# Optimization experiments

Measured on AMD Instinct MI355X. Metric: run time of the kernel, lower is better.

## Reference

```python
import jax, jax.numpy as jnp
import numpy as np

B, S, D = 2, 2048, 768
H, DK, F = 12, 64, 3072
LN_EPS = 1e-5


def setup_inputs() -> dict:
    key = jax.random.key(0)
    ks = jax.random.split(key, 8)
    w = lambda k, shape: jax.random.normal(k, shape, dtype=jnp.float32) * 0.02
    return {
        "x": jax.random.normal(ks[0], (B, S, D), dtype=jnp.float32),
        "wq_w": w(ks[1], (H, D, DK)), "wq_b": jnp.zeros((H, DK), jnp.float32),
        "wk_w": w(ks[2], (H, D, DK)), "wk_b": jnp.zeros((H, DK), jnp.float32),
        "wv_w": w(ks[3], (H, D, DK)), "wv_b": jnp.zeros((H, DK), jnp.float32),
        "wo_w": w(ks[4], (H * DK, D)), "wo_b": jnp.zeros((D,), jnp.float32),
        "ln_g": jnp.ones((D,), jnp.float32), "ln_b": jnp.zeros((D,), jnp.float32),
        "w1": w(ks[5], (D, F)), "b1": jnp.zeros((F,), jnp.float32),
        "w2": w(ks[6], (F, D)), "b2": jnp.zeros((D,), jnp.float32),
    }


def layer_norm(x, g, b):
    mu = jnp.mean(x, axis=-1, keepdims=True)
    var = jnp.mean(jnp.square(x - mu), axis=-1, keepdims=True)
    return (x - mu) * jax.lax.rsqrt(var + LN_EPS) * g + b


def reference(x, wq_w, wq_b, wk_w, wk_b, wv_w, wv_b, wo_w, wo_b,
              ln_g, ln_b, w1, b1, w2, b2):
    dk = wq_w.shape[-1]
    x_res = x
    h = layer_norm(x, ln_b=ln_b, g=ln_g, b=ln_b) if False else layer_norm(x, ln_g, ln_b)
    # per-head QKV (all heads batched via einsum): [B,H,S,DK]
    q = jnp.einsum("bsd,hdk->bhsk", h, wq_w) + wq_b[None, :, None, :]
    k = jnp.einsum("bsd,hdk->bhsk", h, wk_w) + wk_b[None, :, None, :]
    v = jnp.einsum("bsd,hdk->bhsk", h, wv_w) + wv_b[None, :, None, :]
    scores = jnp.einsum("bhqk,bhsk->bhqs", q, k) / jnp.sqrt(jnp.float32(dk))
    attn = jax.nn.softmax(scores, axis=-1)
    o = jnp.einsum("bhqs,bhsk->bhqk", attn, v)  # [B,H,S,DK]
    Bx, Hx, Sx, Dkx = o.shape
    o = o.transpose(0, 2, 1, 3).reshape(Bx, Sx, Hx * Dkx)  # concat heads
    y = o @ wo_w + wo_b + x_res  # residual 1
    y_res = y
    z = layer_norm(y, ln_g, ln_b)
    z = jax.nn.gelu(z @ w1 + b1, approximate=False) @ w2 + b2
    return z + y_res
```

## Files before the change

### kernel.cpp

```cpp
#include <hip/hip_runtime.h>
#include <hip/hip_bf16.h>
#include <math.h>

typedef __bf16 bf16_t;
typedef __bf16 bf16x8 __attribute__((ext_vector_type(8)));
typedef __bf16 bf16x4 __attribute__((ext_vector_type(4)));
typedef float f32x4 __attribute__((ext_vector_type(4)));

#define MFMA_B16(a, b, c) __builtin_amdgcn_mfma_f32_16x16x32_bf16((a), (b), (c), 0, 0, 0)

static constexpr int Bn = 2, Sn = 2048, Dn = 768, Hn = 12, Fn = 3072;
static constexpr int NTOK = Bn * Sn;
#define QSCALE 0.18033688011112042f

__device__ __forceinline__ void gl_lds16(const bf16_t* g, void* lds) {
  __builtin_amdgcn_global_load_lds(
      (const __attribute__((address_space(1))) uint32_t*)g,
      (__attribute__((address_space(3))) uint32_t*)lds, 16, 0, 0);
}

__global__ __launch_bounds__(256) void k_prep(const float* __restrict__ wq, const float* __restrict__ wk,
                                              const float* __restrict__ wv, const float* __restrict__ wo,
                                              const float* __restrict__ w1, const float* __restrict__ w2,
                                              const float* __restrict__ bq, const float* __restrict__ bk,
                                              const float* __restrict__ bv,
                                              bf16_t* __restrict__ WqkvT, bf16_t* __restrict__ WoT,
                                              bf16_t* __restrict__ W1T, bf16_t* __restrict__ W2T,
                                              float* __restrict__ QKVB) {
  int t = blockIdx.x;
  if (t >= 1728) {
    for (int i = threadIdx.x; i < 2304; i += 256)
      QKVB[i] = i < 768 ? bq[i] : (i < 1536 ? bk[i - 768] : bv[i - 1536]);
    return;
  }
  __shared__ float T[64][65];
  const float* src;
  bf16_t* dst;
  int P, Q, tp, tq;
  if (t < 432) {
    int pb = t / 12; tp = t - pb * 12; tq = 0;
    int proj = pb / 12, head = pb - proj * 12;
    src = (proj == 0 ? wq : proj == 1 ? wk : wv) + (size_t)head * 768 * 64;
    dst = WqkvT + (size_t)proj * 589824 + (size_t)head * 64 * 768;
    P = 768; Q = 64;
  } else if (t < 576) {
    int u = t - 432; tp = u / 12; tq = u - tp * 12;
    src = wo; dst = WoT; P = 768; Q = 768;
  } else if (t < 1152) {
    int u = t - 576; tp = u / 48; tq = u - tp * 48;
    src = w1; dst = W1T; P = 768; Q = 3072;
  } else {
    int u = t - 1152; tp = u / 12; tq = u - tp * 12;
    src = w2; dst = W2T; P = 3072; Q = 768;
  }
  int j = threadIdx.x & 63, i0 = threadIdx.x >> 6;
#pragma unroll
  for (int i = i0; i < 64; i += 4)
    T[i][j] = src[(size_t)(tp * 64 + i) * Q + tq * 64 + j];
  __syncthreads();
#pragma unroll
  for (int i = i0; i < 64; i += 4)
    dst[(size_t)(tq * 64 + i) * P + tp * 64 + j] = (bf16_t)T[j][i];
}

__global__ __launch_bounds__(256) void k_layernorm(const float* __restrict__ x,
                                                   const float* __restrict__ g,
                                                   const float* __restrict__ bb,
                                                   bf16_t* __restrict__ out) {
  int t = blockIdx.x, tid = threadIdx.x;
  const float* xr = x + (size_t)t * Dn;
  float v0 = xr[tid], v1 = xr[tid + 256], v2 = xr[tid + 512];
  float s = v0 + v1 + v2;
  float ss = v0 * v0 + v1 * v1 + v2 * v2;
  __shared__ float red[8];
#pragma unroll
  for (int off = 32; off > 0; off >>= 1) {
    s += __shfl_down(s, off);
    ss += __shfl_down(ss, off);
  }
  int w = tid >> 6, l = tid & 63;
  if (l == 0) { red[w] = s; red[4 + w] = ss; }
  __syncthreads();
  s = red[0] + red[1] + red[2] + red[3];
  ss = red[4] + red[5] + red[6] + red[7];
  float mu = s * (1.0f / Dn);
  float var = ss * (1.0f / Dn) - mu * mu;
  float rstd = rsqrtf(var + 1e-5f);
  bf16_t* orow = out + (size_t)t * Dn;
  orow[tid]       = (bf16_t)((v0 - mu) * rstd * g[tid]       + bb[tid]);
  orow[tid + 256] = (bf16_t)((v1 - mu) * rstd * g[tid + 256] + bb[tid + 256]);
  orow[tid + 512] = (bf16_t)((v2 - mu) * rstd * g[tid + 512] + bb[tid + 512]);
}

enum { EPI_QK = 0, EPI_VT = 1, EPI_Y = 2, EPI_GELU = 3, EPI_OUT = 4 };

template <int MT, int NT, int BK, int EPI, int OCC, int SWZ>
__global__ __launch_bounds__(256, OCC) void k_gemm(const bf16_t* __restrict__ A,
                                                   const bf16_t* __restrict__ Bt,
                                                   int N, int K,
                                                   const float* __restrict__ bias,
                                                   const float* __restrict__ resid,
                                                   void* __restrict__ out0,
                                                   void* __restrict__ out1) {
  constexpr int MI = MT / 32, NI = NT / 32;
  constexpr int WROWS = MT / 2, WCOLS = NT / 2;
  constexpr int KS = BK / 32;
  __shared__ __align__(16) bf16_t As[2][MT * BK];
  __shared__ __align__(16) bf16_t Bs[2][NT * BK];
  const int tid = threadIdx.x;
  const int w = tid >> 6, l = tid & 63;
  const int wm = w >> 1, wn = w & 1;
  const int mloc = l & 15, kblk = l >> 4;
  int bx = blockIdx.x, by = blockIdx.y;
  if constexpr (SWZ) {
    int lin = by * gridDim.x + bx;
    int xcd = lin & 7, s = lin >> 3;
    by = xcd * (gridDim.y >> 3) + s / gridDim.x;
    bx = s - (s / gridDim.x) * gridDim.x;
  }

  f32x4 acc[MI][NI];
#pragma unroll
  for (int i = 0; i < MI; ++i)
#pragma unroll
    for (int j = 0; j < NI; ++j) acc[i][j] = f32x4{0.f, 0.f, 0.f, 0.f};

  const bf16_t* gA = A + (size_t)(by * MT + (tid >> 2)) * K + (tid & 3) * 8;
  const bf16_t* gB = Bt + (size_t)(bx * NT + (tid >> 2)) * K + (tid & 3) * 8;
  const int nk = K / BK;

  auto stage = [&](int kt, int buf) {
#pragma unroll
    for (int h = 0; h < KS; ++h) {
#pragma unroll
      for (int rb = 0; rb < MT / 64; ++rb)
        gl_lds16(gA + (size_t)rb * 64 * K + kt * BK + h * 32,
                 (char*)&As[buf][0] + h * (MT * 64) + rb * 4096 + w * 1024);
#pragma unroll
      for (int rb = 0; rb < NT / 64; ++rb)
        gl_lds16(gB + (size_t)rb * 64 * K + kt * BK + h * 32,
                 (char*)&Bs[buf][0] + h * (NT * 64) + rb * 4096 + w * 1024);
    }
  };

  stage(0, 0);
  for (int kt = 0; kt < nk; ++kt) {
    __syncthreads();
    if (kt + 1 < nk) stage(kt + 1, (kt + 1) & 1);
    const bf16_t* Ab = &As[kt & 1][0];
    const bf16_t* Bb = &Bs[kt & 1][0];
    bf16x8 af[MI][KS], bfv[NI][KS];
#pragma unroll
    for (int mi = 0; mi < MI; ++mi)
#pragma unroll
      for (int ks = 0; ks < KS; ++ks)
        af[mi][ks] = *(const bf16x8*)&Ab[ks * (MT * 32) + (wm * WROWS + mi * 16 + mloc) * 32 + kblk * 8];
#pragma unroll
    for (int ni = 0; ni < NI; ++ni)
#pragma unroll
      for (int ks = 0; ks < KS; ++ks)
        bfv[ni][ks] = *(const bf16x8*)&Bb[ks * (NT * 32) + (wn * WCOLS + ni * 16 + mloc) * 32 + kblk * 8];
#pragma unroll
    for (int ks = 0; ks < KS; ++ks)
#pragma unroll
      for (int mi = 0; mi < MI; ++mi)
#pragma unroll
        for (int ni = 0; ni < NI; ++ni)
          acc[mi][ni] = MFMA_B16(af[mi][ks], bfv[ni][ks], acc[mi][ni]);
  }

  const int gmb = by * MT + wm * WROWS + kblk * 4;
  const int gnb = bx * NT + wn * WCOLS + mloc;
  if constexpr (EPI == EPI_QK) {
    constexpr int TPP = 768 / NT;
    const int proj = bx / TPP;
#pragma unroll
    for (int mi = 0; mi < MI; ++mi)
#pragma unroll
      for (int ni = 0; ni < NI; ++ni) {
        int gn = gnb + ni * 16;
        float bv = bias[gn];
        int gm0 = gmb + mi * 16;
        if (proj == 0) {
          bf16_t* dst = (bf16_t*)out0;
#pragma unroll
          for (int r = 0; r < 4; ++r)
            dst[(size_t)(gm0 + r) * 768 + gn] = (bf16_t)((acc[mi][ni][r] + bv) * QSCALE);
        } else {
          bf16_t* dst = (bf16_t*)out1;
#pragma unroll
          for (int r = 0; r < 4; ++r)
            dst[(size_t)(gm0 + r) * 768 + (gn - 768)] = (bf16_t)(acc[mi][ni][r] + bv);
        }
      }
  } else if constexpr (EPI == EPI_VT) {
    bf16_t* dst = (bf16_t*)out0;
#pragma unroll
    for (int mi = 0; mi < MI; ++mi)
#pragma unroll
      for (int ni = 0; ni < NI; ++ni) {
        int gn = gnb + ni * 16;
        int bq = gn >> 11, sq = gn & 2047;
#pragma unroll
        for (int r = 0; r < 4; ++r) {
          int gm = gmb + mi * 16 + r;
          int hq = gm >> 6, dk = gm & 63;
          dst[((size_t)(bq * Hn + hq) * 64 + dk) * Sn + sq] = (bf16_t)(acc[mi][ni][r] + bias[gm]);
        }
      }
  } else if constexpr (EPI == EPI_GELU) {
    bf16_t* dst = (bf16_t*)out0;
#pragma unroll
    for (int mi = 0; mi < MI; ++mi)
#pragma unroll
      for (int ni = 0; ni < NI; ++ni) {
        int gn = gnb + ni * 16;
        float bv = bias[gn];
#pragma unroll
        for (int r = 0; r < 4; ++r) {
          int gm = gmb + mi * 16 + r;
          float t = acc[mi][ni][r] + bv;
          float ge = 0.5f * t * (1.0f + erff(t * 0.70710678118654752f));
          dst[(size_t)gm * N + gn] = (bf16_t)ge;
        }
      }
  } else {
    float* dst = (float*)out0;
#pragma unroll
    for (int mi = 0; mi < MI; ++mi)
#pragma unroll
      for (int ni = 0; ni < NI; ++ni) {
        int gn = gnb + ni * 16;
        float bv = bias[gn];
#pragma unroll
        for (int r = 0; r < 4; ++r) {
          int gm = gmb + mi * 16 + r;
          dst[(size_t)gm * N + gn] = acc[mi][ni][r] + bv + resid[(size_t)gm * N + gn];
        }
      }
  }
}

__global__ __launch_bounds__(256, 2) void k_attn(const bf16_t* __restrict__ Q,
                                                 const bf16_t* __restrict__ K,
                                                 const bf16_t* __restrict__ VT,
                                                 bf16_t* __restrict__ O) {
  __shared__ __align__(16) bf16_t Ks[2][8192];
  __shared__ __align__(16) bf16_t Vs[2][8192];
  const int tid = threadIdx.x, w = tid >> 6, l = tid & 63;
  const int mloc = l & 15, kblk = l >> 4;
  const int bh = blockIdx.y, b = bh / Hn, h = bh - b * Hn;
  const int q0 = blockIdx.x * 64;

  const size_t qoff = (size_t)(b * Sn + q0 + w * 16 + mloc) * Dn + h * 64 + kblk * 8;
  const bf16x8 qf0 = *(const bf16x8*)(Q + qoff);
  const bf16x8 qf1 = *(const bf16x8*)(Q + qoff + 32);

  bf16x8 ones;
#pragma unroll
  for (int j = 0; j < 8; ++j) ones[j] = (bf16_t)1.0f;

  const int tq = tid >> 2, q4 = tid & 3;
  const int s0 = (tq & 0x20) | ((tq & 0x0C) << 1) | ((tq & 0x10) >> 2) | (tq & 3);
  const bf16_t* Kg = K + (size_t)(b * Sn + s0) * Dn + h * 64 + q4 * 8;
  const bf16_t* Vg = VT + ((size_t)bh * 64 + tq) * Sn + q4 * 8;

  f32x4 lacc = f32x4{0.f, 0.f, 0.f, 0.f};
  f32x4 oacc[4];
#pragma unroll
  for (int md = 0; md < 4; ++md) oacc[md] = f32x4{0.f, 0.f, 0.f, 0.f};

  auto stage = [&](int kv0, int buf) {
#pragma unroll
    for (int hh = 0; hh < 2; ++hh) {
      gl_lds16(Kg + (size_t)kv0 * Dn + hh * 32,
               (char*)&Ks[buf][0] + hh * 8192 + w * 1024);
      gl_lds16(Kg + (size_t)(kv0 + 64) * Dn + hh * 32,
               (char*)&Ks[buf][0] + hh * 8192 + 4096 + w * 1024);
    }
#pragma unroll
    for (int c = 0; c < 4; ++c)
      gl_lds16(Vg + kv0 + c * 32,
               (char*)&Vs[buf][0] + c * 4096 + w * 1024);
  };

  stage(0, 0);
  for (int it = 0; it < Sn / 128; ++it) {
    __syncthreads();
    if (it + 1 < Sn / 128) stage((it + 1) * 128, (it + 1) & 1);
    const bf16_t* Kb = &Ks[it & 1][0];
    const bf16_t* Vb = &Vs[it & 1][0];

    f32x4 st[8];
#pragma unroll
    for (int ns = 0; ns < 8; ++ns) {
      const bf16x8 k0 = *(const bf16x8*)&Kb[(ns * 16 + mloc) * 32 + kblk * 8];
      const bf16x8 k1 = *(const bf16x8*)&Kb[4096 + (ns * 16 + mloc) * 32 + kblk * 8];
      f32x4 a = f32x4{0.f, 0.f, 0.f, 0.f};
      a = MFMA_B16(k0, qf0, a);
      a = MFMA_B16(k1, qf1, a);
      st[ns] = a;
    }

    bf16x8 pb[4];
#pragma unroll
    for (int ns = 0; ns < 8; ++ns)
#pragma unroll
      for (int r = 0; r < 4; ++r)
        pb[ns >> 1][(ns & 1) * 4 + r] = (bf16_t)__builtin_amdgcn_exp2f(st[ns][r]);

#pragma unroll
    for (int c = 0; c < 4; ++c) lacc = MFMA_B16(ones, pb[c], lacc);

#pragma unroll
    for (int md = 0; md < 4; ++md)
#pragma unroll
      for (int c = 0; c < 4; ++c) {
        const bf16x8 v = *(const bf16x8*)&Vb[c * 2048 + (md * 16 + mloc) * 32 + kblk * 8];
        oacc[md] = MFMA_B16(v, pb[c], oacc[md]);
      }
  }

  const float inv = 1.0f / lacc[0];
  const size_t obase = (size_t)(b * Sn + q0 + w * 16 + mloc) * Dn + h * 64 + kblk * 4;
#pragma unroll
  for (int md = 0; md < 4; ++md) {
    bf16x4 o4;
#pragma unroll
    for (int r = 0; r < 4; ++r) o4[r] = (bf16_t)(oacc[md][r] * inv);
    *(bf16x4*)&O[obase + md * 16] = o4;
  }
}

extern "C" void kernel_launch(void* const* d_in, const int* in_sizes, int n_in,
                              void* d_out, int out_size, void* d_ws, size_t ws_size,
                              hipStream_t stream) {
  (void)in_sizes; (void)n_in; (void)out_size; (void)ws_size;
  const float* x    = (const float*)d_in[0];
  const float* wq_w = (const float*)d_in[1];
  const float* wq_b = (const float*)d_in[2];
  const float* wk_w = (const float*)d_in[3];
  const float* wk_b = (const float*)d_in[4];
  const float* wv_w = (const float*)d_in[5];
  const float* wv_b = (const float*)d_in[6];
  const float* wo_w = (const float*)d_in[7];
  const float* wo_b = (const float*)d_in[8];
  const float* ln_g = (const float*)d_in[9];
  const float* ln_b = (const float*)d_in[10];
  const float* w1   = (const float*)d_in[11];
  const float* b1   = (const float*)d_in[12];
  const float* w2   = (const float*)d_in[13];
  const float* b2   = (const float*)d_in[14];

  char* ws = (char*)d_ws;
  size_t o = 0;
  bf16_t* WqkvT = (bf16_t*)(ws + o); o += (size_t)2304 * 768 * 2;
  bf16_t* WoT   = (bf16_t*)(ws + o); o += (size_t)768 * 768 * 2;
  bf16_t* W1T   = (bf16_t*)(ws + o); o += (size_t)3072 * 768 * 2;
  bf16_t* W2T   = (bf16_t*)(ws + o); o += (size_t)768 * 3072 * 2;
  float*  QKVB  = (float*)(ws + o);  o += (size_t)2304 * 4;
  bf16_t* Hbuf  = (bf16_t*)(ws + o); o += (size_t)NTOK * 768 * 2;
  bf16_t* Qb    = (bf16_t*)(ws + o); o += (size_t)NTOK * 768 * 2;
  bf16_t* Kb    = (bf16_t*)(ws + o); o += (size_t)NTOK * 768 * 2;
  bf16_t* VbT   = (bf16_t*)(ws + o); o += (size_t)NTOK * 768 * 2;
  float*  Ybuf  = (float*)(ws + o);  o += (size_t)NTOK * 768 * 4;
  bf16_t* Zbuf  = (bf16_t*)(ws + o); o += (size_t)NTOK * 768 * 2;
  bf16_t* Ubuf  = (bf16_t*)(ws + o); o += (size_t)NTOK * 3072 * 2;

  k_prep<<<1729, 256, 0, stream>>>(wq_w, wk_w, wv_w, wo_w, w1, w2,
                                   wq_b, wk_b, wv_b, WqkvT, WoT, W1T, W2T, QKVB);

  k_layernorm<<<NTOK, 256, 0, stream>>>(x, ln_g, ln_b, Hbuf);

  k_gemm<64, 64, 64, EPI_QK, 4, 1><<<dim3(24, 64), 256, 0, stream>>>(Hbuf, WqkvT, 1536, 768,
                                                                     QKVB, nullptr, Qb, Kb);

  k_gemm<64, 64, 64, EPI_VT, 4, 0><<<dim3(64, 12), 256, 0, stream>>>(WqkvT + (size_t)2 * 589824, Hbuf,
                                                                     4096, 768, QKVB + 1536, nullptr,
                                                                     VbT, nullptr);

  k_attn<<<dim3(Sn / 64, Bn * Hn), 256, 0, stream>>>(Qb, Kb, VbT, Hbuf);

  k_gemm<64, 64, 64, EPI_Y, 4, 1><<<dim3(12, 64), 256, 0, stream>>>(Hbuf, WoT, 768, 768,
                                                                    wo_b, x, Ybuf, nullptr);

  k_layernorm<<<NTOK, 256, 0, stream>>>(Ybuf, ln_g, ln_b, Zbuf);

  k_gemm<128, 128, 32, EPI_GELU, 3, 1><<<dim3(24, 32), 256, 0, stream>>>(Zbuf, W1T, 3072, 768,
                                                                         b1, nullptr, Ubuf, nullptr);

  k_gemm<64, 64, 64, EPI_OUT, 4, 1><<<dim3(12, 64), 256, 0, stream>>>(Ubuf, W2T, 768, 3072,
                                                                      b2, Ybuf, d_out, nullptr);
}
```

Before: 288.1 us.

## Fuse first layernorm into prep, enlarge QK GEMM tile, share KV tiles across 8-wave attention

```diff
diff --git a/kernel.cpp b/kernel.cpp
--- a/kernel.cpp
+++ b/kernel.cpp
@@ -26,10 +26,39 @@
                                               const float* __restrict__ bv,
                                               bf16_t* __restrict__ WqkvT, bf16_t* __restrict__ WoT,
                                               bf16_t* __restrict__ W1T, bf16_t* __restrict__ W2T,
-                                              float* __restrict__ QKVB) {
+                                              float* __restrict__ QKVB,
+                                              const float* __restrict__ x, const float* __restrict__ ln_g,
+                                              const float* __restrict__ ln_b, bf16_t* __restrict__ Hbuf) {
   int t = blockIdx.x;
-  if (t >= 1728) {
-    for (int i = threadIdx.x; i < 2304; i += 256)
+  int tid = threadIdx.x;
+  if (t >= 1729) {
+    int tok = t - 1729;
+    const float* xr = x + (size_t)tok * Dn;
+    float v0 = xr[tid], v1 = xr[tid + 256], v2 = xr[tid + 512];
+    float s = v0 + v1 + v2;
+    float ss = v0 * v0 + v1 * v1 + v2 * v2;
+    __shared__ float red[8];
+#pragma unroll
+    for (int off = 32; off > 0; off >>= 1) {
+      s += __shfl_down(s, off);
+      ss += __shfl_down(ss, off);
+    }
+    int w = tid >> 6, l = tid & 63;
+    if (l == 0) { red[w] = s; red[4 + w] = ss; }
+    __syncthreads();
+    s = red[0] + red[1] + red[2] + red[3];
+    ss = red[4] + red[5] + red[6] + red[7];
+    float mu = s * (1.0f / Dn);
+    float var = ss * (1.0f / Dn) - mu * mu;
+    float rstd = rsqrtf(var + 1e-5f);
+    bf16_t* orow = Hbuf + (size_t)tok * Dn;
+    orow[tid]       = (bf16_t)((v0 - mu) * rstd * ln_g[tid]       + ln_b[tid]);
+    orow[tid + 256] = (bf16_t)((v1 - mu) * rstd * ln_g[tid + 256] + ln_b[tid + 256]);
+    orow[tid + 512] = (bf16_t)((v2 - mu) * rstd * ln_g[tid + 512] + ln_b[tid + 512]);
+    return;
+  }
+  if (t == 1728) {
+    for (int i = tid; i < 2304; i += 256)
       QKVB[i] = i < 768 ? bq[i] : (i < 1536 ? bk[i - 768] : bv[i - 1536]);
     return;
   }
@@ -53,7 +82,7 @@
     int u = t - 1152; tp = u / 12; tq = u - tp * 12;
     src = w2; dst = W2T; P = 3072; Q = 768;
   }
-  int j = threadIdx.x & 63, i0 = threadIdx.x >> 6;
+  int j = tid & 63, i0 = tid >> 6;
 #pragma unroll
   for (int i = i0; i < 64; i += 4)
     T[i][j] = src[(size_t)(tp * 64 + i) * Q + tq * 64 + j];
@@ -241,7 +270,7 @@
   }
 }
 
-__global__ __launch_bounds__(256, 2) void k_attn(const bf16_t* __restrict__ Q,
+__global__ __launch_bounds__(512, 2) void k_attn(const bf16_t* __restrict__ Q,
                                                  const bf16_t* __restrict__ K,
                                                  const bf16_t* __restrict__ VT,
                                                  bf16_t* __restrict__ O) {
@@ -250,9 +279,10 @@
   const int tid = threadIdx.x, w = tid >> 6, l = tid & 63;
   const int mloc = l & 15, kblk = l >> 4;
   const int bh = blockIdx.y, b = bh / Hn, h = bh - b * Hn;
-  const int q0 = blockIdx.x * 64;
-
-  const size_t qoff = (size_t)(b * Sn + q0 + w * 16 + mloc) * Dn + h * 64 + kblk * 8;
+  const int q0 = blockIdx.x * 128 + (w >> 2) * 64;
+  const int wq = w & 3;
+
+  const size_t qoff = (size_t)(b * Sn + q0 + wq * 16 + mloc) * Dn + h * 64 + kblk * 8;
   const bf16x8 qf0 = *(const bf16x8*)(Q + qoff);
   const bf16x8 qf1 = *(const bf16x8*)(Q + qoff + 32);
 
@@ -261,9 +291,11 @@
   for (int j = 0; j < 8; ++j) ones[j] = (bf16_t)1.0f;
 
   const int tq = tid >> 2, q4 = tid & 3;
-  const int s0 = (tq & 0x20) | ((tq & 0x0C) << 1) | ((tq & 0x10) >> 2) | (tq & 3);
+  const int s0 = (tq & 0x60) | ((tq & 0x0C) << 1) | ((tq & 0x10) >> 2) | (tq & 3);
   const bf16_t* Kg = K + (size_t)(b * Sn + s0) * Dn + h * 64 + q4 * 8;
-  const bf16_t* Vg = VT + ((size_t)bh * 64 + tq) * Sn + q4 * 8;
+  const int code0 = 2 * w, code1 = 2 * w + 1;
+  const bf16_t* Vg0 = VT + ((size_t)bh * 64 + (code0 & 3) * 16 + (l >> 2)) * Sn + (code0 >> 2) * 32 + (l & 3) * 8;
+  const bf16_t* Vg1 = VT + ((size_t)bh * 64 + (code1 & 3) * 16 + (l >> 2)) * Sn + (code1 >> 2) * 32 + (l & 3) * 8;
 
   f32x4 lacc = f32x4{0.f, 0.f, 0.f, 0.f};
   f32x4 oacc[4];
@@ -271,17 +303,10 @@
   for (int md = 0; md < 4; ++md) oacc[md] = f32x4{0.f, 0.f, 0.f, 0.f};
 
   auto stage = [&](int kv0, int buf) {
-#pragma unroll
-    for (int hh = 0; hh < 2; ++hh) {
-      gl_lds16(Kg + (size_t)kv0 * Dn + hh * 32,
-               (char*)&Ks[buf][0] + hh * 8192 + w * 1024);
-      gl_lds16(Kg + (size_t)(kv0 + 64) * Dn + hh * 32,
-               (char*)&Ks[buf][0] + hh * 8192 + 4096 + w * 1024);
-    }
-#pragma unroll
-    for (int c = 0; c < 4; ++c)
-      gl_lds16(Vg + kv0 + c * 32,
-               (char*)&Vs[buf][0] + c * 4096 + w * 1024);
+    gl_lds16(Kg + (size_t)kv0 * Dn,      (char*)&Ks[buf][0] + w * 1024);
+    gl_lds16(Kg + (size_t)kv0 * Dn + 32, (char*)&Ks[buf][0] + 8192 + w * 1024);
+    gl_lds16(Vg0 + kv0, (char*)&Vs[buf][0] + w * 2048);
+    gl_lds16(Vg1 + kv0, (char*)&Vs[buf][0] + w * 2048 + 1024);
   };
 
   stage(0, 0);
@@ -322,7 +347,7 @@
   }
 
   const float inv = 1.0f / lacc[0];
-  const size_t obase = (size_t)(b * Sn + q0 + w * 16 + mloc) * Dn + h * 64 + kblk * 4;
+  const size_t obase = (size_t)(b * Sn + q0 + wq * 16 + mloc) * Dn + h * 64 + kblk * 4;
 #pragma unroll
   for (int md = 0; md < 4; ++md) {
     bf16x4 o4;
@@ -367,19 +392,18 @@
   bf16_t* Zbuf  = (bf16_t*)(ws + o); o += (size_t)NTOK * 768 * 2;
   bf16_t* Ubuf  = (bf16_t*)(ws + o); o += (size_t)NTOK * 3072 * 2;
 
-  k_prep<<<1729, 256, 0, stream>>>(wq_w, wk_w, wv_w, wo_w, w1, w2,
-                                   wq_b, wk_b, wv_b, WqkvT, WoT, W1T, W2T, QKVB);
-
-  k_layernorm<<<NTOK, 256, 0, stream>>>(x, ln_g, ln_b, Hbuf);
-
-  k_gemm<64, 64, 64, EPI_QK, 4, 1><<<dim3(24, 64), 256, 0, stream>>>(Hbuf, WqkvT, 1536, 768,
-                                                                     QKVB, nullptr, Qb, Kb);
+  k_prep<<<1729 + NTOK, 256, 0, stream>>>(wq_w, wk_w, wv_w, wo_w, w1, w2,
+                                          wq_b, wk_b, wv_b, WqkvT, WoT, W1T, W2T, QKVB,
+                                          x, ln_g, ln_b, Hbuf);
+
+  k_gemm<128, 64, 64, EPI_QK, 3, 1><<<dim3(24, 32), 256, 0, stream>>>(Hbuf, WqkvT, 1536, 768,
+                                                                      QKVB, nullptr, Qb, Kb);
 
   k_gemm<64, 64, 64, EPI_VT, 4, 0><<<dim3(64, 12), 256, 0, stream>>>(WqkvT + (size_t)2 * 589824, Hbuf,
                                                                      4096, 768, QKVB + 1536, nullptr,
                                                                      VbT, nullptr);
 
-  k_attn<<<dim3(Sn / 64, Bn * Hn), 256, 0, stream>>>(Qb, Kb, VbT, Hbuf);
+  k_attn<<<dim3(Sn / 128, Bn * Hn), 512, 0, stream>>>(Qb, Kb, VbT, Hbuf);
 
   k_gemm<64, 64, 64, EPI_Y, 4, 1><<<dim3(12, 64), 256, 0, stream>>>(Hbuf, WoT, 768, 768,
                                                                     wo_b, x, Ybuf, nullptr);
```

After: 271.2 us. 5.9% less time.
